# Performance work log

Measured on AMD Instinct MI355X. Metric: run time of the kernel, lower is better.

The kernel has to match this reference:

```python
import jax, jax.numpy as jnp
import numpy as np

VOCAB = 50000
EMBED = 256
LABELS = 2
DEPTH = 10          # complete binary tree: 2**DEPTH leaves
B = 256             # batch of trees
L = 2 ** DEPTH      # leaves per tree


def setup_inputs() -> dict:
    key = jax.random.key(0)
    ks = jax.random.split(key, 7)
    token_ids = jax.random.randint(ks[0], (B, L), 0, VOCAB)
    labels = jax.random.randint(ks[1], (B,), 0, LABELS)
    emb = jax.random.normal(ks[2], (VOCAB, EMBED), dtype=jnp.float32)
    W_w = jax.random.normal(ks[3], (EMBED, 2 * EMBED), dtype=jnp.float32) * (1.0 / np.sqrt(2 * EMBED))
    W_b = jax.random.normal(ks[4], (EMBED,), dtype=jnp.float32) * 0.01
    P_w = jax.random.normal(ks[5], (LABELS, EMBED), dtype=jnp.float32) * (1.0 / np.sqrt(EMBED))
    P_b = jax.random.normal(ks[6], (LABELS,), dtype=jnp.float32) * 0.01
    return {"token_ids": token_ids, "labels": labels, "emb": emb,
            "W_w": W_w, "W_b": W_b, "P_w": P_w, "P_b": P_b}


def reference(token_ids, labels, emb, W_w, W_b, P_w, P_b):
    # Leaves: relu(embedding(token))  -> [B, L, E]
    x = jax.nn.relu(emb[token_ids])
    # Level-by-level combine: currentNode = relu(W @ cat(left, right) + b)
    # Leaf order is left-to-right, so adjacent pairs (2k, 2k+1) are siblings;
    # reshape concatenates (left, right) along features, matching torch.cat((l, r), 1).
    while x.shape[1] > 1:
        bsz, n, e = x.shape
        lr = x.reshape(bsz, n // 2, 2 * e)                       # [B, n/2, 2E]
        x = jax.nn.relu(jnp.einsum('bnf,ef->bne', lr, W_w) + W_b)
    root = x[:, 0]                                               # [B, E]
    logits = root @ P_w.T + P_b                                  # [B, label_size]
    prediction = jnp.argmax(logits, axis=1)
    logp = jax.nn.log_softmax(logits, axis=-1)
    loss = -jnp.take_along_axis(logp, labels[:, None], axis=1)[:, 0]  # per-tree CE
    return prediction, loss
```

## Files before the change

### kernel.cpp

```cpp
#include <hip/hip_runtime.h>
#include <hip/hip_bf16.h>
#include <math.h>

#define EMBED   256
#define KDIM    512
#define BATCH   256
#define BM      128
#define VOCAB   50000

typedef float  f32x4   __attribute__((ext_vector_type(4)));
typedef __bf16 bf16x8  __attribute__((ext_vector_type(8)));
typedef unsigned short ushort8 __attribute__((ext_vector_type(8)));

__device__ __forceinline__ unsigned short f2h(float f) {
    unsigned int u = __float_as_uint(f);
    u += 0x7FFFu + ((u >> 16) & 1u);
    return (unsigned short)(u >> 16);
}
__device__ __forceinline__ float h2f(unsigned short h) {
    return __uint_as_float(((unsigned int)h) << 16);
}
__device__ __forceinline__ void gload16(const void* g, void* l) {
    __builtin_amdgcn_global_load_lds(
        (const __attribute__((address_space(1))) unsigned int*)g,
        (__attribute__((address_space(3))) unsigned int*)l, 16, 0, 0);
}

__global__ __launch_bounds__(256) void prep_all(const float* __restrict__ emb,
                                                unsigned short* __restrict__ Eh,
                                                unsigned short* __restrict__ El,
                                                const float* __restrict__ W,
                                                unsigned short* __restrict__ Wh,
                                                unsigned short* __restrict__ Wl,
                                                int wprep)
{
    const int bid = blockIdx.x;
    if (bid < 6250) {
        const size_t base = ((size_t)bid * 256 + threadIdx.x) * 8;
        float v[8];
        *(float4*)&v[0] = *(const float4*)&emb[base];
        *(float4*)&v[4] = *(const float4*)&emb[base + 4];
        ushort8 hs, ls;
        #pragma unroll
        for (int i = 0; i < 8; ++i) {
            const float f = fmaxf(v[i], 0.f);
            const unsigned short h = f2h(f);
            hs[i] = h;
            ls[i] = f2h(f - h2f(h));
        }
        *(ushort8*)&Eh[base] = hs;
        *(ushort8*)&El[base] = ls;
    } else if (wprep) {
        const int i = (bid - 6250) * 256 + threadIdx.x;
        const float w = W[i];
        const unsigned short h = f2h(w);
        Wh[i] = h;
        Wl[i] = f2h(w - h2f(h));
    }
}

template<int LV1>
__global__ __launch_bounds__(512) void gemm_pipe(
    const unsigned short* __restrict__ Xh, const unsigned short* __restrict__ Xl,
    const unsigned short* __restrict__ Wh, const unsigned short* __restrict__ Wl,
    const float*  __restrict__ bias,
    unsigned short* __restrict__ Yh, unsigned short* __restrict__ Yl,
    const int* __restrict__ tok,
    const unsigned short* __restrict__ Eh, const unsigned short* __restrict__ El)
{
    __shared__ __align__(16) unsigned short AhL[3][4096], AlL[3][4096];
    __shared__ __align__(16) unsigned short BhL[3][8192], BlL[3][8192];

    const int tid = threadIdx.x;
    const int wid = tid >> 6;
    const int l   = tid & 63;
    const int q   = l >> 4;
    const int rr  = l & 15;
    const int m0  = blockIdx.x * BM;

    const int waveM = wid >> 2;
    const int waveN = wid & 3;

    int tk0 = 0, tk1 = 0;
    if constexpr (LV1) {
        const int r = m0 + wid * 16 + rr;
        tk0 = tok[2 * r];
        tk1 = tok[2 * r + 1];
    }

    auto stage = [&](int buf, int t) {
        const int k0   = t << 5;
        const int joff = k0 >> 8;
        const int c    = (k0 & 255) + q * 8;
        if constexpr (LV1) {
            const size_t off = (size_t)(joff ? tk1 : tk0) * EMBED + c;
            gload16(Eh + off, &AhL[buf][wid * 512]);
            gload16(El + off, &AlL[buf][wid * 512]);
        } else {
            const size_t off = (size_t)(2 * (m0 + wid * 16 + rr) + joff) * EMBED + c;
            gload16(Xh + off, &AhL[buf][wid * 512]);
            gload16(Xl + off, &AlL[buf][wid * 512]);
        }
        #pragma unroll
        for (int g = 0; g < 2; ++g) {
            const int s = wid + g * 8;
            const size_t woff = (size_t)(s * 16 + rr) * KDIM + k0 + q * 8;
            gload16(Wh + woff, &BhL[buf][s * 512]);
            gload16(Wl + woff, &BlL[buf][s * 512]);
        }
    };

    f32x4 acc[4][4] = {};

    stage(0, 0);
    stage(1, 1);
    stage(2, 2);
    asm volatile("s_waitcnt vmcnt(12)" ::: "memory");
    __builtin_amdgcn_sched_barrier(0);
    __builtin_amdgcn_s_barrier();
    __builtin_amdgcn_sched_barrier(0);

    int cur = 0;
    for (int t = 0; t < 16; ++t) {
        bf16x8 ah[4], al[4], bh[4], bl[4];
        #pragma unroll
        for (int mi = 0; mi < 4; ++mi) {
            ah[mi] = *(const bf16x8*)&AhL[cur][(waveM * 4 + mi) * 512 + l * 8];
            al[mi] = *(const bf16x8*)&AlL[cur][(waveM * 4 + mi) * 512 + l * 8];
        }
        #pragma unroll
        for (int ni = 0; ni < 4; ++ni) {
            bh[ni] = *(const bf16x8*)&BhL[cur][(waveN * 4 + ni) * 512 + l * 8];
            bl[ni] = *(const bf16x8*)&BlL[cur][(waveN * 4 + ni) * 512 + l * 8];
        }
        asm volatile("s_waitcnt lgkmcnt(0)" ::: "memory");
        __builtin_amdgcn_sched_barrier(0);
        __builtin_amdgcn_s_barrier();
        __builtin_amdgcn_sched_barrier(0);

        if (t + 3 < 16) stage(cur, t + 3);

        __builtin_amdgcn_s_setprio(1);
        #pragma unroll
        for (int mi = 0; mi < 4; ++mi)
            #pragma unroll
            for (int ni = 0; ni < 4; ++ni)
                acc[mi][ni] = __builtin_amdgcn_mfma_f32_16x16x32_bf16(ah[mi], bh[ni], acc[mi][ni], 0, 0, 0);
        #pragma unroll
        for (int mi = 0; mi < 4; ++mi)
            #pragma unroll
            for (int ni = 0; ni < 4; ++ni)
                acc[mi][ni] = __builtin_amdgcn_mfma_f32_16x16x32_bf16(al[mi], bh[ni], acc[mi][ni], 0, 0, 0);
        #pragma unroll
        for (int mi = 0; mi < 4; ++mi)
            #pragma unroll
            for (int ni = 0; ni < 4; ++ni)
                acc[mi][ni] = __builtin_amdgcn_mfma_f32_16x16x32_bf16(ah[mi], bl[ni], acc[mi][ni], 0, 0, 0);
        __builtin_amdgcn_s_setprio(0);

        if (t < 15) {
            if (t <= 12)      { asm volatile("s_waitcnt vmcnt(12)" ::: "memory"); }
            else if (t == 13) { asm volatile("s_waitcnt vmcnt(6)"  ::: "memory"); }
            else              { asm volatile("s_waitcnt vmcnt(0)"  ::: "memory"); }
            __builtin_amdgcn_sched_barrier(0);
            __builtin_amdgcn_s_barrier();
            __builtin_amdgcn_sched_barrier(0);
        }
        cur = (cur == 2) ? 0 : cur + 1;
    }

    #pragma unroll
    for (int ni = 0; ni < 4; ++ni) {
        const int col = waveN * 64 + ni * 16 + rr;
        const float bv = bias[col];
        #pragma unroll
        for (int mi = 0; mi < 4; ++mi) {
            const int row0 = m0 + waveM * 64 + mi * 16 + q * 4;
            #pragma unroll
            for (int jj = 0; jj < 4; ++jj) {
                const float y = fmaxf(acc[mi][ni][jj] + bv, 0.f);
                const unsigned short h = f2h(y);
                Yh[(size_t)(row0 + jj) * EMBED + col] = h;
                Yl[(size_t)(row0 + jj) * EMBED + col] = f2h(y - h2f(h));
            }
        }
    }
}

template<int LV1>
__global__ __launch_bounds__(512) void gemm_tree(
    const unsigned short* __restrict__ Xh, const unsigned short* __restrict__ Xl,
    const float*  __restrict__ Wf,
    const float*  __restrict__ bias,
    unsigned short* __restrict__ Yh, unsigned short* __restrict__ Yl,
    const int* __restrict__ tok,
    const unsigned short* __restrict__ Eh, const unsigned short* __restrict__ El)
{
    __shared__ __align__(16) unsigned short AhL[4096], AlL[4096];
    __shared__ __align__(16) unsigned short BhL[8192], BlL[8192];

    const int tid = threadIdx.x;
    const int wid = tid >> 6;
    const int l   = tid & 63;
    const int q   = l >> 4;
    const int rr  = l & 15;
    const int m0  = blockIdx.x * BM;
    const int waveM = wid >> 2;
    const int waveN = wid & 3;

    int tk0 = 0, tk1 = 0;
    if constexpr (LV1) {
        const int r = m0 + wid * 16 + rr;
        tk0 = tok[2 * r];
        tk1 = tok[2 * r + 1];
    }

    f32x4 acc[4][4] = {};

    for (int t = 0; t < 16; ++t) {
        const int k0   = t << 5;
        const int joff = k0 >> 8;
        const int c    = (k0 & 255) + q * 8;

        if constexpr (LV1) {
            const size_t off = (size_t)(joff ? tk1 : tk0) * EMBED + c;
            gload16(Eh + off, &AhL[wid * 512]);
            gload16(El + off, &AlL[wid * 512]);
        } else {
            const size_t off = (size_t)(2 * (m0 + wid * 16 + rr) + joff) * EMBED + c;
            gload16(Xh + off, &AhL[wid * 512]);
            gload16(Xl + off, &AlL[wid * 512]);
        }
        #pragma unroll
        for (int g = 0; g < 2; ++g) {
            const int s = wid + g * 8;
            const float* ws = Wf + (size_t)(s * 16 + rr) * KDIM + k0 + q * 8;
            float v[8];
            *(float4*)&v[0] = *(const float4*)ws;
            *(float4*)&v[4] = *(const float4*)(ws + 4);
            ushort8 hs, ls;
            #pragma unroll
            for (int i = 0; i < 8; ++i) {
                const unsigned short h = f2h(v[i]);
                hs[i] = h;
                ls[i] = f2h(v[i] - h2f(h));
            }
            *(ushort8*)&BhL[s * 512 + l * 8] = hs;
            *(ushort8*)&BlL[s * 512 + l * 8] = ls;
        }
        __syncthreads();

        bf16x8 ah[4], al[4], bh[4], bl[4];
        #pragma unroll
        for (int mi = 0; mi < 4; ++mi) {
            ah[mi] = *(const bf16x8*)&AhL[(waveM * 4 + mi) * 512 + l * 8];
            al[mi] = *(const bf16x8*)&AlL[(waveM * 4 + mi) * 512 + l * 8];
        }
        #pragma unroll
        for (int ni = 0; ni < 4; ++ni) {
            bh[ni] = *(const bf16x8*)&BhL[(waveN * 4 + ni) * 512 + l * 8];
            bl[ni] = *(const bf16x8*)&BlL[(waveN * 4 + ni) * 512 + l * 8];
        }
        #pragma unroll
        for (int mi = 0; mi < 4; ++mi)
            #pragma unroll
            for (int ni = 0; ni < 4; ++ni)
                acc[mi][ni] = __builtin_amdgcn_mfma_f32_16x16x32_bf16(ah[mi], bh[ni], acc[mi][ni], 0, 0, 0);
        #pragma unroll
        for (int mi = 0; mi < 4; ++mi)
            #pragma unroll
            for (int ni = 0; ni < 4; ++ni)
                acc[mi][ni] = __builtin_amdgcn_mfma_f32_16x16x32_bf16(al[mi], bh[ni], acc[mi][ni], 0, 0, 0);
        #pragma unroll
        for (int mi = 0; mi < 4; ++mi)
            #pragma unroll
            for (int ni = 0; ni < 4; ++ni)
                acc[mi][ni] = __builtin_amdgcn_mfma_f32_16x16x32_bf16(ah[mi], bl[ni], acc[mi][ni], 0, 0, 0);

        __syncthreads();
    }

    #pragma unroll
    for (int ni = 0; ni < 4; ++ni) {
        const int col = waveN * 64 + ni * 16 + rr;
        const float bv = bias[col];
        #pragma unroll
        for (int mi = 0; mi < 4; ++mi) {
            const int row0 = m0 + waveM * 64 + mi * 16 + q * 4;
            #pragma unroll
            for (int jj = 0; jj < 4; ++jj) {
                const float y = fmaxf(acc[mi][ni][jj] + bv, 0.f);
                const unsigned short h = f2h(y);
                Yh[(size_t)(row0 + jj) * EMBED + col] = h;
                Yl[(size_t)(row0 + jj) * EMBED + col] = f2h(y - h2f(h));
            }
        }
    }
}

template<int WPREP>
__global__ __launch_bounds__(256) void tail_kernel(
    const unsigned short* __restrict__ A4h, const unsigned short* __restrict__ A4l,
    const unsigned short* __restrict__ Wh, const unsigned short* __restrict__ Wl,
    const float* __restrict__ Wf, const float* __restrict__ bias,
    const float* __restrict__ Pw, const float* __restrict__ Pb,
    const int* __restrict__ labels, float* __restrict__ out)
{
    __shared__ __align__(16) unsigned short X0h[8192], X0l[8192];
    __shared__ __align__(16) unsigned short X1h[4096], X1l[4096];
    __shared__ __align__(16) unsigned short BhT[2][8192], BlT[2][8192];
    __shared__ __align__(16) unsigned short Asth[2][1024], Astl[2][1024];

    const int tid = threadIdx.x;
    const int w   = tid >> 6;
    const int l   = tid & 63;
    const int q   = l >> 4;
    const int rr  = l & 15;
    const int b   = blockIdx.x;

    auto stageB = [&](int buf, int k0) {
        if constexpr (WPREP) {
            #pragma unroll
            for (int j = 0; j < 8; ++j) {
                const int sb = w * 8 + j;
                const int s  = sb & 15;
                const size_t off = (size_t)(s * 16 + rr) * KDIM + k0 + q * 8;
                if (sb < 16) gload16(Wh + off, &BhT[buf][s * 512]);
                else         gload16(Wl + off, &BlT[buf][s * 512]);
            }
        } else {
            #pragma unroll
            for (int j = 0; j < 4; ++j) {
                const int u = w * 4 + j;
                const float* ws = Wf + (size_t)(u * 16 + rr) * KDIM + k0 + q * 8;
                float v[8];
                *(float4*)&v[0] = *(const float4*)ws;
                *(float4*)&v[4] = *(const float4*)(ws + 4);
                ushort8 hs, ls;
                #pragma unroll
                for (int i = 0; i < 8; ++i) {
                    const unsigned short h = f2h(v[i]);
                    hs[i] = h;
                    ls[i] = f2h(v[i] - h2f(h));
                }
                *(ushort8*)&BhT[buf][u * 512 + l * 8] = hs;
                *(ushort8*)&BlT[buf][u * 512 + l * 8] = ls;
            }
        }
    };

    auto stageA = [&](int buf, int t) {
        if (w < 2) {
            const int k0   = t * 32;
            const int joff = k0 >> 8;
            const int c    = (k0 & 255) + q * 8;
            const size_t off = (size_t)(64 * b + 2 * (w * 16 + rr) + joff) * EMBED + c;
            gload16(A4h + off, &Asth[buf][w * 512]);
            gload16(A4l + off, &Astl[buf][w * 512]);
        }
    };

    float bv[4];
    #pragma unroll
    for (int ni = 0; ni < 4; ++ni) bv[ni] = bias[w * 64 + ni * 16 + rr];

    stageB(0, 0);
    stageA(0, 0);
    __syncthreads();

    int g = 0;
    for (int s = 0; s < 6; ++s) {
        unsigned short* srch = (s & 1) ? X0h : X1h;
        unsigned short* srcl = (s & 1) ? X0l : X1l;
        unsigned short* dsth = (s & 1) ? X1h : X0h;
        unsigned short* dstl = (s & 1) ? X1l : X0l;
        const int Mout = 32 >> s;

        f32x4 acc[2][4] = {};
        for (int t = 0; t < 16; ++t, ++g) {
            const int cur = g & 1;
            if (g < 95) stageB(cur ^ 1, ((t + 1) & 15) * 32);
            if (s == 0 && t < 15) stageA(cur ^ 1, t + 1);

            const int k0   = t * 32;
            const int joff = k0 >> 8;
            const int c    = (k0 & 255) + q * 8;

            bf16x8 a_h0, a_l0;
            if (s == 0) {
                a_h0 = *(const bf16x8*)&Asth[cur][l * 8];
                a_l0 = *(const bf16x8*)&Astl[cur][l * 8];
            } else {
                const int row = 2 * rr + joff;
                const int idx = (row * 256 + c) ^ ((row & 7) << 3);
                a_h0 = *(const bf16x8*)&srch[idx];
                a_l0 = *(const bf16x8*)&srcl[idx];
            }

            bf16x8 bh4[4], bl4[4];
            #pragma unroll
            for (int ni = 0; ni < 4; ++ni) {
                bh4[ni] = *(const bf16x8*)&BhT[cur][(w * 4 + ni) * 512 + l * 8];
                bl4[ni] = *(const bf16x8*)&BlT[cur][(w * 4 + ni) * 512 + l * 8];
            }
            #pragma unroll
            for (int ni = 0; ni < 4; ++ni)
                acc[0][ni] = __builtin_amdgcn_mfma_f32_16x16x32_bf16(a_h0, bh4[ni], acc[0][ni], 0, 0, 0);
            #pragma unroll
            for (int ni = 0; ni < 4; ++ni)
                acc[0][ni] = __builtin_amdgcn_mfma_f32_16x16x32_bf16(a_l0, bh4[ni], acc[0][ni], 0, 0, 0);
            #pragma unroll
            for (int ni = 0; ni < 4; ++ni)
                acc[0][ni] = __builtin_amdgcn_mfma_f32_16x16x32_bf16(a_h0, bl4[ni], acc[0][ni], 0, 0, 0);

            if (s == 0) {
                const bf16x8 a_h1 = *(const bf16x8*)&Asth[cur][512 + l * 8];
                const bf16x8 a_l1 = *(const bf16x8*)&Astl[cur][512 + l * 8];
                #pragma unroll
                for (int ni = 0; ni < 4; ++ni)
                    acc[1][ni] = __builtin_amdgcn_mfma_f32_16x16x32_bf16(a_h1, bh4[ni], acc[1][ni], 0, 0, 0);
                #pragma unroll
                for (int ni = 0; ni < 4; ++ni)
                    acc[1][ni] = __builtin_amdgcn_mfma_f32_16x16x32_bf16(a_l1, bh4[ni], acc[1][ni], 0, 0, 0);
                #pragma unroll
                for (int ni = 0; ni < 4; ++ni)
                    acc[1][ni] = __builtin_amdgcn_mfma_f32_16x16x32_bf16(a_h1, bl4[ni], acc[1][ni], 0, 0, 0);
            }
            __syncthreads();
        }

        #pragma unroll
        for (int ni = 0; ni < 4; ++ni) {
            const int col = w * 64 + ni * 16 + rr;
            #pragma unroll
            for (int jj = 0; jj < 4; ++jj) {
                const int row = q * 4 + jj;
                if (row < Mout) {
                    const float y = fmaxf(acc[0][ni][jj] + bv[ni], 0.f);
                    const unsigned short h = f2h(y);
                    const int idx = (row * 256 + col) ^ ((row & 7) << 3);
                    dsth[idx] = h;
                    dstl[idx] = f2h(y - h2f(h));
                }
            }
            if (s == 0) {
                #pragma unroll
                for (int jj = 0; jj < 4; ++jj) {
                    const int row = 16 + q * 4 + jj;
                    const float y = fmaxf(acc[1][ni][jj] + bv[ni], 0.f);
                    const unsigned short h = f2h(y);
                    const int idx = (row * 256 + col) ^ ((row & 7) << 3);
                    dsth[idx] = h;
                    dstl[idx] = f2h(y - h2f(h));
                }
            }
        }
        __syncthreads();
    }

    if (w == 0) {
        float s0 = 0.f, s1 = 0.f;
        #pragma unroll
        for (int i = 0; i < 4; ++i) {
            const int col = l + i * 64;
            const float x = h2f(X1h[col]) + h2f(X1l[col]);
            s0 = fmaf(x, Pw[col], s0);
            s1 = fmaf(x, Pw[EMBED + col], s1);
        }
        #pragma unroll
        for (int off = 32; off > 0; off >>= 1) {
            s0 += __shfl_down(s0, off);
            s1 += __shfl_down(s1, off);
        }
        if (l == 0) {
            const float l0 = s0 + Pb[0];
            const float l1 = s1 + Pb[1];
            const int pred = (l1 > l0) ? 1 : 0;
            const float m  = fmaxf(l0, l1);
            const float lse = m + logf(expf(l0 - m) + expf(l1 - m));
            const int lab = labels[b];
            out[b]         = (float)pred;
            out[BATCH + b] = lse - (lab ? l1 : l0);
        }
    }
}

extern "C" void kernel_launch(void* const* d_in, const int* in_sizes, int n_in,
                              void* d_out, int out_size, void* d_ws, size_t ws_size,
                              hipStream_t stream)
{
    const int*   token_ids = (const int*)d_in[0];
    const int*   labels    = (const int*)d_in[1];
    const float* emb       = (const float*)d_in[2];
    const float* W_w       = (const float*)d_in[3];
    const float* W_b       = (const float*)d_in[4];
    const float* P_w       = (const float*)d_in[5];
    const float* P_b       = (const float*)d_in[6];
    float*       out       = (float*)d_out;

    unsigned short* Ah_buf = (unsigned short*)d_ws;
    unsigned short* Al_buf = Ah_buf + (size_t)131072 * 256;
    unsigned short* Bh_buf = Al_buf + (size_t)131072 * 256;
    unsigned short* Bl_buf = Bh_buf + (size_t)65536 * 256;
    unsigned short* Wh     = Bl_buf + (size_t)65536 * 256;
    unsigned short* Wl     = Wh + 131072;
    unsigned short* Eh     = Bh_buf;
    unsigned short* El     = Bl_buf;

    const size_t need_wprep = ((size_t)131072 * 256 * 2 + (size_t)65536 * 256 * 2 + 2 * 131072) * 2;
    const bool wprep = ws_size >= need_wprep;

    prep_all<<<6762, 256, 0, stream>>>(emb, Eh, El, W_w, Wh, Wl, wprep ? 1 : 0);

    if (wprep) {
        gemm_pipe<1><<<1024, 512, 0, stream>>>(nullptr, nullptr, Wh, Wl, W_b, Ah_buf, Al_buf, token_ids, Eh, El);
        gemm_pipe<0><<< 512, 512, 0, stream>>>(Ah_buf, Al_buf, Wh, Wl, W_b, Bh_buf, Bl_buf, nullptr, nullptr, nullptr);
        gemm_pipe<0><<< 256, 512, 0, stream>>>(Bh_buf, Bl_buf, Wh, Wl, W_b, Ah_buf, Al_buf, nullptr, nullptr, nullptr);
        gemm_pipe<0><<< 128, 512, 0, stream>>>(Ah_buf, Al_buf, Wh, Wl, W_b, Bh_buf, Bl_buf, nullptr, nullptr, nullptr);
        tail_kernel<1><<<BATCH, 256, 0, stream>>>(Bh_buf, Bl_buf, Wh, Wl, W_w, W_b, P_w, P_b, labels, out);
    } else {
        gemm_tree<1><<<1024, 512, 0, stream>>>(nullptr, nullptr, W_w, W_b, Ah_buf, Al_buf, token_ids, Eh, El);
        gemm_tree<0><<< 512, 512, 0, stream>>>(Ah_buf, Al_buf, W_w, W_b, Bh_buf, Bl_buf, nullptr, nullptr, nullptr);
        gemm_tree<0><<< 256, 512, 0, stream>>>(Bh_buf, Bl_buf, W_w, W_b, Ah_buf, Al_buf, nullptr, nullptr, nullptr);
        gemm_tree<0><<< 128, 512, 0, stream>>>(Ah_buf, Al_buf, W_w, W_b, Bh_buf, Bl_buf, nullptr, nullptr, nullptr);
        tail_kernel<0><<<BATCH, 256, 0, stream>>>(Bh_buf, Bl_buf, Wh, Wl, W_w, W_b, P_w, P_b, labels, out);
    }
}
```

Before: 471.6 us.

## Load W fragments directly from global into registers, shrink tile to 64 rows

The level GEMM kernel drops LDS staging of the weight matrix. Each wave now reads its B fragments (hi/lo bf16) straight from global memory into registers, and only the activation tile goes through a triple-buffered LDS pipeline. Block size is halved to 256 threads with a 64-row M tile, so grids double and the LDS footprint is much smaller, which allows higher occupancy. The cost is more global/L2 traffic for W, since each block re-reads the full weight slice, and barrier and vmcnt handling is reorganised around the new load ordering.

```diff
diff --git a/kernel.cpp b/kernel.cpp
--- a/kernel.cpp
+++ b/kernel.cpp
@@ -60,7 +60,7 @@
 }
 
 template<int LV1>
-__global__ __launch_bounds__(512) void gemm_pipe(
+__global__ __launch_bounds__(256) void gemm_bpipe(
     const unsigned short* __restrict__ Xh, const unsigned short* __restrict__ Xl,
     const unsigned short* __restrict__ Wh, const unsigned short* __restrict__ Wl,
     const float*  __restrict__ bias,
@@ -68,77 +68,78 @@
     const int* __restrict__ tok,
     const unsigned short* __restrict__ Eh, const unsigned short* __restrict__ El)
 {
-    __shared__ __align__(16) unsigned short AhL[3][4096], AlL[3][4096];
-    __shared__ __align__(16) unsigned short BhL[3][8192], BlL[3][8192];
+    __shared__ __align__(16) unsigned short AhL[3][2048], AlL[3][2048];
 
     const int tid = threadIdx.x;
-    const int wid = tid >> 6;
+    const int w   = tid >> 6;
     const int l   = tid & 63;
     const int q   = l >> 4;
     const int rr  = l & 15;
-    const int m0  = blockIdx.x * BM;
-
-    const int waveM = wid >> 2;
-    const int waveN = wid & 3;
+    const int m0  = blockIdx.x * 64;
 
     int tk0 = 0, tk1 = 0;
     if constexpr (LV1) {
-        const int r = m0 + wid * 16 + rr;
+        const int r = m0 + w * 16 + rr;
         tk0 = tok[2 * r];
         tk1 = tok[2 * r + 1];
     }
 
-    auto stage = [&](int buf, int t) {
+    auto stageA = [&](int buf, int t) {
         const int k0   = t << 5;
         const int joff = k0 >> 8;
         const int c    = (k0 & 255) + q * 8;
         if constexpr (LV1) {
             const size_t off = (size_t)(joff ? tk1 : tk0) * EMBED + c;
-            gload16(Eh + off, &AhL[buf][wid * 512]);
-            gload16(El + off, &AlL[buf][wid * 512]);
+            gload16(Eh + off, &AhL[buf][w * 512]);
+            gload16(El + off, &AlL[buf][w * 512]);
         } else {
-            const size_t off = (size_t)(2 * (m0 + wid * 16 + rr) + joff) * EMBED + c;
-            gload16(Xh + off, &AhL[buf][wid * 512]);
-            gload16(Xl + off, &AlL[buf][wid * 512]);
-        }
-        #pragma unroll
-        for (int g = 0; g < 2; ++g) {
-            const int s = wid + g * 8;
-            const size_t woff = (size_t)(s * 16 + rr) * KDIM + k0 + q * 8;
-            gload16(Wh + woff, &BhL[buf][s * 512]);
-            gload16(Wl + woff, &BlL[buf][s * 512]);
+            const size_t off = (size_t)(2 * (m0 + w * 16 + rr) + joff) * EMBED + c;
+            gload16(Xh + off, &AhL[buf][w * 512]);
+            gload16(Xl + off, &AlL[buf][w * 512]);
         }
     };
 
     f32x4 acc[4][4] = {};
 
-    stage(0, 0);
-    stage(1, 1);
-    stage(2, 2);
-    asm volatile("s_waitcnt vmcnt(12)" ::: "memory");
-    __builtin_amdgcn_sched_barrier(0);
-    __builtin_amdgcn_s_barrier();
-    __builtin_amdgcn_sched_barrier(0);
-
-    int cur = 0;
+    stageA(0, 0);
+    stageA(1, 1);
+    stageA(2, 2);
+
     for (int t = 0; t < 16; ++t) {
-        bf16x8 ah[4], al[4], bh[4], bl[4];
+        const int k0   = t << 5;
+        const int bufi = t % 3;
+
+        bf16x8 bh[4], bl[4];
+        #pragma unroll
+        for (int ni = 0; ni < 4; ++ni) {
+            const size_t boff = (size_t)(w * 64 + ni * 16 + rr) * KDIM + k0 + q * 8;
+            bh[ni] = *(const bf16x8*)&Wh[boff];
+            bl[ni] = *(const bf16x8*)&Wl[boff];
+        }
+
+        asm volatile("s_waitcnt vmcnt(12)" ::: "memory");
+        __builtin_amdgcn_sched_barrier(0);
+        __builtin_amdgcn_s_barrier();
+        __builtin_amdgcn_sched_barrier(0);
+
+        bf16x8 ah[4], al[4];
         #pragma unroll
         for (int mi = 0; mi < 4; ++mi) {
-            ah[mi] = *(const bf16x8*)&AhL[cur][(waveM * 4 + mi) * 512 + l * 8];
-            al[mi] = *(const bf16x8*)&AlL[cur][(waveM * 4 + mi) * 512 + l * 8];
-        }
-        #pragma unroll
-        for (int ni = 0; ni < 4; ++ni) {
-            bh[ni] = *(const bf16x8*)&BhL[cur][(waveN * 4 + ni) * 512 + l * 8];
-            bl[ni] = *(const bf16x8*)&BlL[cur][(waveN * 4 + ni) * 512 + l * 8];
+            ah[mi] = *(const bf16x8*)&AhL[bufi][mi * 512 + l * 8];
+            al[mi] = *(const bf16x8*)&AlL[bufi][mi * 512 + l * 8];
         }
         asm volatile("s_waitcnt lgkmcnt(0)" ::: "memory");
         __builtin_amdgcn_sched_barrier(0);
         __builtin_amdgcn_s_barrier();
         __builtin_amdgcn_sched_barrier(0);
 
-        if (t + 3 < 16) stage(cur, t + 3);
+        if (t + 3 < 16) {
+            stageA(bufi, t + 3);
+            asm volatile("s_waitcnt vmcnt(2)" ::: "memory");
+        } else {
+            asm volatile("s_waitcnt vmcnt(0)" ::: "memory");
+        }
+        __builtin_amdgcn_sched_barrier(0);
 
         __builtin_amdgcn_s_setprio(1);
         #pragma unroll
@@ -157,25 +158,15 @@
             for (int ni = 0; ni < 4; ++ni)
                 acc[mi][ni] = __builtin_amdgcn_mfma_f32_16x16x32_bf16(ah[mi], bl[ni], acc[mi][ni], 0, 0, 0);
         __builtin_amdgcn_s_setprio(0);
-
-        if (t < 15) {
-            if (t <= 12)      { asm volatile("s_waitcnt vmcnt(12)" ::: "memory"); }
-            else if (t == 13) { asm volatile("s_waitcnt vmcnt(6)"  ::: "memory"); }
-            else              { asm volatile("s_waitcnt vmcnt(0)"  ::: "memory"); }
-            __builtin_amdgcn_sched_barrier(0);
-            __builtin_amdgcn_s_barrier();
-            __builtin_amdgcn_sched_barrier(0);
-        }
-        cur = (cur == 2) ? 0 : cur + 1;
     }
 
     #pragma unroll
     for (int ni = 0; ni < 4; ++ni) {
-        const int col = waveN * 64 + ni * 16 + rr;
+        const int col = w * 64 + ni * 16 + rr;
         const float bv = bias[col];
         #pragma unroll
         for (int mi = 0; mi < 4; ++mi) {
-            const int row0 = m0 + waveM * 64 + mi * 16 + q * 4;
+            const int row0 = m0 + mi * 16 + q * 4;
             #pragma unroll
             for (int jj = 0; jj < 4; ++jj) {
                 const float y = fmaxf(acc[mi][ni][jj] + bv, 0.f);
@@ -513,10 +504,10 @@
     prep_all<<<6762, 256, 0, stream>>>(emb, Eh, El, W_w, Wh, Wl, wprep ? 1 : 0);
 
     if (wprep) {
-        gemm_pipe<1><<<1024, 512, 0, stream>>>(nullptr, nullptr, Wh, Wl, W_b, Ah_buf, Al_buf, token_ids, Eh, El);
-        gemm_pipe<0><<< 512, 512, 0, stream>>>(Ah_buf, Al_buf, Wh, Wl, W_b, Bh_buf, Bl_buf, nullptr, nullptr, nullptr);
-        gemm_pipe<0><<< 256, 512, 0, stream>>>(Bh_buf, Bl_buf, Wh, Wl, W_b, Ah_buf, Al_buf, nullptr, nullptr, nullptr);
-        gemm_pipe<0><<< 128, 512, 0, stream>>>(Ah_buf, Al_buf, Wh, Wl, W_b, Bh_buf, Bl_buf, nullptr, nullptr, nullptr);
+        gemm_bpipe<1><<<2048, 256, 0, stream>>>(nullptr, nullptr, Wh, Wl, W_b, Ah_buf, Al_buf, token_ids, Eh, El);
+        gemm_bpipe<0><<<1024, 256, 0, stream>>>(Ah_buf, Al_buf, Wh, Wl, W_b, Bh_buf, Bl_buf, nullptr, nullptr, nullptr);
+        gemm_bpipe<0><<< 512, 256, 0, stream>>>(Bh_buf, Bl_buf, Wh, Wl, W_b, Ah_buf, Al_buf, nullptr, nullptr, nullptr);
+        gemm_bpipe<0><<< 256, 256, 0, stream>>>(Ah_buf, Al_buf, Wh, Wl, W_b, Bh_buf, Bl_buf, nullptr, nullptr, nullptr);
         tail_kernel<1><<<BATCH, 256, 0, stream>>>(Bh_buf, Bl_buf, Wh, Wl, W_w, W_b, P_w, P_b, labels, out);
     } else {
         gemm_tree<1><<<1024, 512, 0, stream>>>(nullptr, nullptr, W_w, W_b, Ah_buf, Al_buf, token_ids, Eh, El);
```

Result: slower. 486.1 us (+3.1%).
